# Kernel optimization log

Hardware: AMD Instinct MI355X
Metric: run time of the kernel (lower is better)

Reference implementation:

```python
import jax, jax.numpy as jnp
import numpy as np

MIN_VAL = 1e-10


def integ_exp_trig(lam, theta, t, t0=None):
    # Analytic integrals of exp(lam*s)*cos(theta*s) and exp(lam*s)*sin(theta*s) on [t0, t].
    if t0 is None:
        t0 = jnp.zeros_like(t)
    exps_t = jnp.nan_to_num(jnp.exp(lam * t))
    exps_t0 = jnp.nan_to_num(jnp.exp(lam * t0))
    denom = jnp.square(lam) + jnp.square(theta)
    scale = jnp.sign(denom) / jnp.clip(denom, MIN_VAL)
    cos_t, sin_t = jnp.cos(theta * t), jnp.sin(theta * t)
    cos_t0, sin_t0 = jnp.cos(theta * t0), jnp.sin(theta * t0)
    res_cos = scale * (exps_t * (lam * cos_t + theta * sin_t)
                       - exps_t0 * (lam * cos_t0 + theta * sin_t0))
    res_sin = scale * (exps_t * (lam * sin_t - theta * cos_t)
                       - exps_t0 * (lam * sin_t0 - theta * cos_t0))
    return jnp.nan_to_num(res_cos), jnp.nan_to_num(res_sin)


def esde_predict_complex(X0, X0_var, U, times, Q, lam_real, lam_imag, V_real, V_imag):
    B, n = X0.shape
    m = n // 2
    lam = lam_real + 1j * lam_imag          # [B, m] complex
    V = V_real + 1j * V_imag                # [B, n, m] complex
    X0c = X0[:, :, None]                    # [B, n, 1]

    # Phi(0): exp(0*lam) = 1, so phi_comp = V
    Phi0 = jnp.concatenate([V.real, V.imag], axis=2)        # [B, n, n]
    Phi0_inv = jnp.nan_to_num(jnp.linalg.inv(Phi0))

    init_cond = Phi0_inv @ X0c                               # [B, n, 1]
    init_var = Phi0_inv @ X0_var @ jnp.swapaxes(Phi0_inv, -1, -2)

    # Phi(t)
    et = jnp.exp(times[:, None].astype(lam.dtype) * lam)     # [B, m] complex
    phi = V * et[:, None, :]                                 # right-mult by diag(et)
    Phi = jnp.nan_to_num(jnp.concatenate([phi.real, phi.imag], axis=2))  # [B, n, n]

    Hom = Phi @ init_cond
    Hom_var = Phi @ init_var @ jnp.swapaxes(Phi, -1, -2)
    # force positive diagonal: diag -> |diag|, off-diag unchanged
    eye = jnp.eye(n, dtype=Hom_var.dtype)
    diag_sign = jnp.sign(jnp.diagonal(Hom_var, axis1=-2, axis2=-1))  # [B, n]
    Hom_var = Hom_var * ((1.0 - eye) + eye * diag_sign[:, :, None])

    # ----- particular (control) term: block 2x2 rotation-integral times Phi0_inv @ U
    ext_u = (Phi0_inv @ U[:, :, None]).reshape(B, m, 2)      # interleaved (re, im) pairs
    cos_int, sin_int = integ_exp_trig(-lam.real, lam.imag, times[:, None])  # [B, m]
    li0 = cos_int * ext_u[..., 0] - sin_int * ext_u[..., 1]
    li1 = sin_int * ext_u[..., 0] + cos_int * ext_u[..., 1]
    lambda_int = jnp.stack([li0, li1], axis=-1).reshape(B, n, 1)
    Part = Phi @ lambda_int

    # ----- diffusion variance term
    ext_s = Phi0_inv @ Q @ jnp.swapaxes(Phi0_inv, -1, -2)    # [B, n, n]
    ls = lam[:, None, :] + lam[:, :, None]                   # lam_i + lam_j
    ls_conj = lam[:, None, :] - lam[:, :, None]              # lam_j - lam_i
    t3 = times[:, None, None]
    cos1, sin1 = integ_exp_trig(-ls.real, ls.imag, t3)       # [B, m, m]
    cos2, sin2 = integ_exp_trig(-ls.real, ls_conj.imag, t3)
    vcc = 0.5 * (cos1 + cos2)   # int cos*cos
    vsc = 0.5 * (sin1 + sin2)   # int sin*cos
    vcs = 0.5 * (sin1 - sin2)   # int cos*sin
    vss = 0.5 * (cos2 - cos1)   # int sin*sin
    E = ext_s.reshape(B, m, 2, m, 2)  # interleaved 2x2 block structure
    d11, d12 = E[:, :, 0, :, 0], E[:, :, 0, :, 1]
    d21, d22 = E[:, :, 1, :, 0], E[:, :, 1, :, 1]
    r11 = vcc * d11 - vsc * d21 - vcs * d12 + vss * d22
    r12 = vcs * d11 - vss * d21 + vcc * d12 - vsc * d22
    r21 = vsc * d11 + vcc * d21 - vss * d12 - vcs * d22
    r22 = vss * d11 + vcs * d21 + vsc * d12 + vcc * d22
    row0 = jnp.stack([r11, r12], axis=-1)   # [B, m, m, 2]
    row1 = jnp.stack([r21, r22], axis=-1)
    sig_int = jnp.stack([row0, row1], axis=2).reshape(B, n, n)
    Part_var = Phi @ sig_int @ jnp.swapaxes(Phi, -1, -2)

    return Hom + Part, Hom_var + Part_var


def setup_inputs() -> dict:
    key = jax.random.key(0)
    ks = jax.random.split(key, 9)
    B, n = 65536, 16
    m = n // 2
    X0 = jax.random.normal(ks[0], (B, n), jnp.float32)
    A = jax.random.normal(ks[1], (B, n, n), jnp.float32) * 0.1
    X0_var = A @ jnp.swapaxes(A, -1, -2) + 0.1 * jnp.eye(n, dtype=jnp.float32)
    U = jax.random.normal(ks[2], (B, n), jnp.float32)
    times = jax.random.uniform(ks[3], (B,), jnp.float32, 0.1, 2.0)
    Qa = jax.random.normal(ks[4], (B, n, n), jnp.float32) * 0.1
    Q = Qa @ jnp.swapaxes(Qa, -1, -2)
    lam_real = -jax.random.uniform(ks[5], (B, m), jnp.float32, 0.05, 1.0)
    lam_imag = jax.random.uniform(ks[6], (B, m), jnp.float32, -2.0, 2.0)
    V_real = jax.random.normal(ks[7], (B, n, m), jnp.float32)
    V_imag = jax.random.normal(ks[8], (B, n, m), jnp.float32)
    return {"X0": X0, "X0_var": X0_var, "U": U, "times": times, "Q": Q,
            "lam_real": lam_real, "lam_imag": lam_imag,
            "V_real": V_real, "V_imag": V_imag}


def reference(X0, X0_var, U, times, Q, lam_real, lam_imag, V_real, V_imag):
    return esde_predict_complex(X0, X0_var, U, times, Q,
                                lam_real, lam_imag, V_real, V_imag)
```

## Files before the change

kernel.cpp:

```cpp
#include <hip/hip_runtime.h>
#include <math.h>

#define WSYNC() do { __builtin_amdgcn_wave_barrier(); asm volatile("" ::: "memory"); } while (0)
#define LFENCE() asm volatile("" ::: "memory")

constexpr int FS = 20;

typedef float v2f __attribute__((ext_vector_type(2)));
__device__ inline v2f pkfma(v2f a, v2f b, v2f c) {
  return __builtin_elementwise_fma(a, b, c);
}

struct alignas(16) WaveMem {
  float P[16 * FS];
  float F[16 * FS];
  float W[16 * FS];
  float L1[16 * FS];
  float L4[16 * FS];
  float etr[8], eti[8], lamr[8], lami[8];
  float vx0[16], vu[16], vic[16];
};

__device__ inline float n2n(float v) {
  if (isnan(v)) return 0.0f;
  if (isinf(v)) return v > 0.f ? 3.402823466e38f : -3.402823466e38f;
  return v;
}

__device__ inline float readlane_f(float v, int l) {
  return __int_as_float(__builtin_amdgcn_readlane(__float_as_int(v), l));
}
template<int CTRL>
__device__ inline float dpp_f(float v) {
  return __int_as_float(__builtin_amdgcn_mov_dpp(__float_as_int(v), CTRL, 0xF, 0xF, true));
}

__device__ inline void load16(float out[16], const float* p) {
#pragma unroll
  for (int c = 0; c < 4; ++c) {
    float4 v = *(const float4*)(p + 4 * c);
    out[4*c+0] = v.x; out[4*c+1] = v.y; out[4*c+2] = v.z; out[4*c+3] = v.w;
  }
}

template<bool TRB>
__device__ inline void mmv(float* C, const float* A, const float* Bm,
                           int i16, int jg, bool absdiag = false)
{
  const int j0 = jg << 2;
  float aA[16];
  load16(aA, &A[i16 * FS]);
  float acc[4];
  if (TRB) {
#pragma unroll
    for (int cp = 0; cp < 2; ++cp) {
      float bB0[16], bB1[16];
      load16(bB0, &Bm[(j0 + 2*cp) * FS]);
      load16(bB1, &Bm[(j0 + 2*cp + 1) * FS]);
      v2f s = {0.f, 0.f};
#pragma unroll
      for (int k = 0; k < 16; ++k)
        s = pkfma((v2f){aA[k], aA[k]}, (v2f){bB0[k], bB1[k]}, s);
      acc[2*cp] = s.x; acc[2*cp+1] = s.y;
    }
  } else {
    v2f a01 = {0.f, 0.f}, a23 = {0.f, 0.f};
#pragma unroll
    for (int k = 0; k < 16; ++k) {
      float4 bv = *(const float4*)&Bm[k * FS + j0];
      v2f ad = {aA[k], aA[k]};
      a01 = pkfma(ad, (v2f){bv.x, bv.y}, a01);
      a23 = pkfma(ad, (v2f){bv.z, bv.w}, a23);
    }
    acc[0] = a01.x; acc[1] = a01.y; acc[2] = a23.x; acc[3] = a23.y;
  }
  if (absdiag) {
#pragma unroll
    for (int c = 0; c < 4; ++c) if (i16 == j0 + c) acc[c] = fabsf(acc[c]);
  }
  *(float4*)&C[i16 * FS + j0] = make_float4(acc[0], acc[1], acc[2], acc[3]);
}

__global__ __launch_bounds__(256, 6) void nesde_kernel(
    const float* __restrict__ gX0, const float* __restrict__ gXv,
    const float* __restrict__ gU,  const float* __restrict__ gT,
    const float* __restrict__ gQ,  const float* __restrict__ gLr,
    const float* __restrict__ gLi, const float* __restrict__ gVr,
    const float* __restrict__ gVi, float* __restrict__ gOut0,
    float* __restrict__ gOut1, int B)
{
  __shared__ WaveMem sm[4];
  const int wid  = threadIdx.x >> 6;
  const int lane = threadIdx.x & 63;
  const int b = blockIdx.x * 4 + wid;
  if (b >= B) return;
  WaveMem& S = sm[wid];

  const int r4  = lane >> 2;
  const int q   = lane & 3;
  const int i16 = lane & 15;
  const int jg  = lane >> 4;
  const int j0  = jg << 2;

  const float t = gT[b];

  const float4 xv = *(const float4*)(gXv + (size_t)b * 256 + lane * 4);
  const float4 qv = *(const float4*)(gQ  + (size_t)b * 256 + lane * 4);
  float4 va = make_float4(0.f,0.f,0.f,0.f), vb = va;
  if (q < 2) {
    const float* src = (q == 0) ? gVr : gVi;
    va = *(const float4*)(src + (size_t)b * 128 + r4 * 8);
    vb = *(const float4*)(src + (size_t)b * 128 + r4 * 8 + 4);
  }
  float x0u = 0.f;
  if (q == 2) x0u = gX0[(size_t)b * 16 + r4];
  if (q == 3) x0u = gU [(size_t)b * 16 + r4];

  if (lane < 8) {
    float lr = gLr[(size_t)b * 8 + lane];
    float li = gLi[(size_t)b * 8 + lane];
    S.lamr[lane] = lr; S.lami[lane] = li;
    float e = expf(lr * t);
    float sn, cs; sincosf(li * t, &sn, &cs);
    S.etr[lane] = e * cs;
    S.eti[lane] = e * sn;
  }
  WSYNC();

  float4 vco;
  {
    const int p = lane >> 3, qq = lane & 7;
    float la  = -(S.lamr[p] + S.lamr[qq]);
    float th1 = S.lami[p] + S.lami[qq];
    float th2 = S.lami[qq] - S.lami[p];
    float exps = __expf(la * t);
    float s1, c1, s2, c2;
    __sincosf(th1 * t, &s1, &c1);
    __sincosf(th2 * t, &s2, &c2);
    float den1 = la * la + th1 * th1;
    float sg1 = (den1 > 0.f) ? 1.f : ((den1 < 0.f) ? -1.f : 0.f);
    float sc1 = sg1 / fmaxf(den1, 1e-10f);
    float cos1 = sc1 * (exps * (la * c1 + th1 * s1) - la);
    float sin1 = sc1 * (exps * (la * s1 - th1 * c1) + th1);
    float den2 = la * la + th2 * th2;
    float sg2 = (den2 > 0.f) ? 1.f : ((den2 < 0.f) ? -1.f : 0.f);
    float sc2 = sg2 / fmaxf(den2, 1e-10f);
    float cos2 = sc2 * (exps * (la * c2 + th2 * s2) - la);
    float sin2 = sc2 * (exps * (la * s2 - th2 * c2) + th2);
    vco = make_float4(0.5f * (cos1 + cos2), 0.5f * (sin1 + sin2),
                      0.5f * (sin1 - sin2), 0.5f * (cos2 - cos1));
  }
  {
    const int si = lane >> 2, sj = (lane & 3) * 4;
    *(float4*)&S.L1[si * FS + sj] = xv;
    *(float4*)&S.L4[si * FS + sj] = qv;
  }
  if (q == 2) S.vx0[r4] = x0u;
  if (q == 3) S.vu[r4]  = x0u;

  float myv[8] = { va.x, va.y, va.z, va.w, vb.x, vb.y, vb.z, vb.w };
  float ov[8];
#pragma unroll
  for (int e = 0; e < 8; ++e) ov[e] = __shfl_xor(myv[e], 1);
  if (q < 2) {
    float er[8], ei[8];
#pragma unroll
    for (int e = 0; e < 8; ++e) { er[e] = S.etr[e]; ei[e] = S.eti[e]; }
    float vr[8], vi[8], ph[8];
#pragma unroll
    for (int e = 0; e < 8; ++e) {
      vr[e] = (q == 0) ? myv[e] : ov[e];
      vi[e] = (q == 0) ? ov[e]  : myv[e];
    }
    if (q == 0) {
#pragma unroll
      for (int e = 0; e < 8; ++e) ph[e] = vr[e] * er[e] - vi[e] * ei[e];
      *(float4*)&S.F[r4 * FS + 0] = make_float4(ph[0], ph[1], ph[2], ph[3]);
      *(float4*)&S.F[r4 * FS + 4] = make_float4(ph[4], ph[5], ph[6], ph[7]);
    } else {
#pragma unroll
      for (int e = 0; e < 8; ++e) ph[e] = vr[e] * ei[e] + vi[e] * er[e];
      *(float4*)&S.F[r4 * FS + 8]  = make_float4(ph[0], ph[1], ph[2], ph[3]);
      *(float4*)&S.F[r4 * FS + 12] = make_float4(ph[4], ph[5], ph[6], ph[7]);
    }
  }

  float a[8];
#pragma unroll
  for (int e = 0; e < 8; ++e) {
    float idv = 0.f;
    if (q == 2) idv = (r4 == e)     ? 1.f : 0.f;
    if (q == 3) idv = (r4 == 8 + e) ? 1.f : 0.f;
    a[e] = (q < 2) ? myv[e] : idv;
  }

  unsigned used = 0;
  int myk = 0;
#pragma unroll
  for (int k = 0; k < 16; ++k) {
    const int qk = k >> 3, ek = k & 7;
    float av = a[ek];
    float ck = (qk == 0) ? dpp_f<0x00>(av) : dpp_f<0x55>(av);
    float cand = ((used >> r4) & 1u) ? -1.0f : fabsf(ck);
    float mx = cand;
    mx = fmaxf(mx, dpp_f<0x124>(mx));
    mx = fmaxf(mx, dpp_f<0x128>(mx));
    mx = fmaxf(mx, dpp_f<0x142>(mx));
    mx = fmaxf(mx, dpp_f<0x143>(mx));
    float smx = readlane_f(mx, 63);
    unsigned long long msk = __ballot(cand == smx);
    const int pl4 = (__ffsll((long long)msk) - 1) & 60;
    const bool isp = ((lane & 60) == pl4);
    if (isp) {
      *(float4*)&S.W[q * 8]     = make_float4(a[0], a[1], a[2], a[3]);
      *(float4*)&S.W[q * 8 + 4] = make_float4(a[4], a[5], a[6], a[7]);
    }
    float pval = readlane_f(av, pl4 | qk);
    float pivinv = 1.0f / pval;
    LFENCE();
    float4 r0 = *(const float4*)&S.W[q * 8];
    float4 r1 = *(const float4*)&S.W[q * 8 + 4];
    LFENCE();
    float rr[8] = { r0.x, r0.y, r0.z, r0.w, r1.x, r1.y, r1.z, r1.w };
    const v2f pivd = { pivinv, pivinv };
    const v2f nck  = { -ck, -ck };
#pragma unroll
    for (int e2 = 0; e2 < 4; ++e2) {
      v2f rrp = { rr[2*e2], rr[2*e2+1] };
      v2f sp  = rrp * pivd;
      v2f up  = pkfma(nck, sp, (v2f){ a[2*e2], a[2*e2+1] });
      a[2*e2]   = isp ? sp.x : up.x;
      a[2*e2+1] = isp ? sp.y : up.y;
    }
    used |= 1u << (pl4 >> 2);
    if (isp) myk = k;
  }

  if (q >= 2) {
    const int base = myk * FS + ((q - 2) << 3);
    *(float4*)&S.P[base]     = make_float4(n2n(a[0]), n2n(a[1]), n2n(a[2]), n2n(a[3]));
    *(float4*)&S.P[base + 4] = make_float4(n2n(a[4]), n2n(a[5]), n2n(a[6]), n2n(a[7]));
  }
  WSYNC();

  if (lane < 32) {
    const float* src = (lane < 16) ? S.vx0 : S.vu;
    float sv[16], pA[16];
    load16(pA, &S.P[i16 * FS]);
    load16(sv, src);
    float d = 0.f;
#pragma unroll
    for (int k = 0; k < 16; ++k) d = fmaf(pA[k], sv[k], d);
    if (lane < 16) S.vic[i16] = d; else S.vu[i16] = d;
  }
  WSYNC();
  if (lane < 8) {
    float la = -S.lamr[lane], th = S.lami[lane];
    float exps = expf(la * t);
    float sn, cs; sincosf(th * t, &sn, &cs);
    float denom = la * la + th * th;
    float sgn = (denom > 0.f) ? 1.f : ((denom < 0.f) ? -1.f : 0.f);
    float scale = sgn / fmaxf(denom, 1e-10f);
    float ci = scale * (exps * (la * cs + th * sn) - la);
    float si = scale * (exps * (la * sn - th * cs) + th);
    float e0 = S.vu[2 * lane], e1 = S.vu[2 * lane + 1];
    S.vic[2 * lane]     += ci * e0 - si * e1;
    S.vic[2 * lane + 1] += si * e0 + ci * e1;
  }
  WSYNC();
  if (lane < 16) {
    float fA[16], vv[16];
    load16(fA, &S.F[lane * FS]);
    load16(vv, S.vic);
    float d = 0.f;
#pragma unroll
    for (int k = 0; k < 16; ++k) d = fmaf(fA[k], vv[k], d);
    gOut0[(size_t)b * 16 + lane] = d;
  }
  WSYNC();

  mmv<false>(S.W,  S.P, S.L4, i16, jg);        WSYNC();
  mmv<true >(S.L4, S.W, S.P,  i16, jg);        WSYNC();
  mmv<false>(S.W,  S.F, S.P,  i16, jg);        WSYNC();
  mmv<false>(S.P,  S.W, S.L1, i16, jg);        WSYNC();
  mmv<true >(S.L1, S.P, S.W,  i16, jg, true);  WSYNC();

  {
    const int p2 = i16 >> 1, aa = i16 & 1;
    const int sA = p2 * 8 + (j0 >> 1);
    float4 c0, c1;
    c0.x = __shfl(vco.x, sA);     c0.y = __shfl(vco.y, sA);
    c0.z = __shfl(vco.z, sA);     c0.w = __shfl(vco.w, sA);
    c1.x = __shfl(vco.x, sA + 1); c1.y = __shfl(vco.y, sA + 1);
    c1.z = __shfl(vco.z, sA + 1); c1.w = __shfl(vco.w, sA + 1);
    float4 top = *(const float4*)&S.L4[(2 * p2) * FS + j0];
    float4 bot = *(const float4*)&S.L4[(2 * p2 + 1) * FS + j0];
    float tl[4] = { top.x, top.y, top.z, top.w };
    float bl[4] = { bot.x, bot.y, bot.z, bot.w };
    float r[4];
#pragma unroll
    for (int uu = 0; uu < 4; ++uu) {
      float4 c = (uu < 2) ? c0 : c1;
      const int off = 2 * (uu >> 1);
      float d11 = tl[off], d12 = tl[off + 1];
      float d21 = bl[off], d22 = bl[off + 1];
      const int bb = uu & 1;
      if (aa == 0)
        r[uu] = (bb == 0) ? (c.x * d11 - c.y * d21 - c.z * d12 + c.w * d22)
                          : (c.z * d11 - c.w * d21 + c.x * d12 - c.y * d22);
      else
        r[uu] = (bb == 0) ? (c.y * d11 + c.x * d21 - c.w * d12 - c.z * d22)
                          : (c.w * d11 + c.z * d21 + c.y * d12 + c.x * d22);
    }
    *(float4*)&S.W[i16 * FS + j0] = make_float4(r[0], r[1], r[2], r[3]);
  }
  WSYNC();
  mmv<false>(S.L4, S.F, S.W, i16, jg);         WSYNC();

  {
    float aA[16];
    load16(aA, &S.L4[i16 * FS]);
    float acc[4];
#pragma unroll
    for (int cp = 0; cp < 2; ++cp) {
      float bB0[16], bB1[16];
      load16(bB0, &S.F[(j0 + 2*cp) * FS]);
      load16(bB1, &S.F[(j0 + 2*cp + 1) * FS]);
      v2f s = {0.f, 0.f};
#pragma unroll
      for (int k = 0; k < 16; ++k)
        s = pkfma((v2f){aA[k], aA[k]}, (v2f){bB0[k], bB1[k]}, s);
      acc[2*cp] = s.x; acc[2*cp+1] = s.y;
    }
    float4 hv = *(const float4*)&S.L1[i16 * FS + j0];
    float4 o = make_float4(hv.x + acc[0], hv.y + acc[1], hv.z + acc[2], hv.w + acc[3]);
    *(float4*)&gOut1[(size_t)b * 256 + i16 * 16 + j0] = o;
  }
}

extern "C" void kernel_launch(void* const* d_in, const int* in_sizes, int n_in,
                              void* d_out, int out_size, void* d_ws, size_t ws_size,
                              hipStream_t stream) {
  const float* X0 = (const float*)d_in[0];
  const float* Xv = (const float*)d_in[1];
  const float* U  = (const float*)d_in[2];
  const float* T  = (const float*)d_in[3];
  const float* Q  = (const float*)d_in[4];
  const float* Lr = (const float*)d_in[5];
  const float* Li = (const float*)d_in[6];
  const float* Vr = (const float*)d_in[7];
  const float* Vi = (const float*)d_in[8];
  const int B = in_sizes[3];
  float* out0 = (float*)d_out;
  float* out1 = (float*)d_out + (size_t)B * 16;
  const int blocks = (B + 3) / 4;
  hipLaunchKernelGGL(nesde_kernel, dim3(blocks), dim3(256), 0, stream,
                     X0, Xv, U, T, Q, Lr, Li, Vr, Vi, out0, out1, B);
}
```

Before: 192.3 us.

## Switch matrix inversion to in-place Gauss-Jordan with 4 columns per lane

Rewrites the per-batch 16x16 inverse. Before, each lane carried 8 entries of an augmented [V|I] matrix. Now each of the four lanes in a row group holds 4 columns and the pivot columns are overwritten in place with the inverse. Pivot positions are recorded in packed nibble masks so the columns can be unpermuted at the final scatter. The V load and the Phi construction are reorganised so that all four lanes do equal work. This halves per-lane register use and FMA work in the elimination loop, at the cost of a scattered scalar store at the end.

```diff
diff --git a/kernel.cpp b/kernel.cpp
--- a/kernel.cpp
+++ b/kernel.cpp
@@ -106,11 +106,10 @@
 
   const float4 xv = *(const float4*)(gXv + (size_t)b * 256 + lane * 4);
   const float4 qv = *(const float4*)(gQ  + (size_t)b * 256 + lane * 4);
-  float4 va = make_float4(0.f,0.f,0.f,0.f), vb = va;
-  if (q < 2) {
-    const float* src = (q == 0) ? gVr : gVi;
-    va = *(const float4*)(src + (size_t)b * 128 + r4 * 8);
-    vb = *(const float4*)(src + (size_t)b * 128 + r4 * 8 + 4);
+  float4 v4;
+  {
+    const float* src = (q < 2) ? gVr : gVi;
+    v4 = *(const float4*)(src + (size_t)b * 128 + r4 * 8 + ((q & 1) << 2));
   }
   float x0u = 0.f;
   if (q == 2) x0u = gX0[(size_t)b * 16 + r4];
@@ -158,49 +157,34 @@
   if (q == 2) S.vx0[r4] = x0u;
   if (q == 3) S.vu[r4]  = x0u;
 
-  float myv[8] = { va.x, va.y, va.z, va.w, vb.x, vb.y, vb.z, vb.w };
-  float ov[8];
-#pragma unroll
-  for (int e = 0; e < 8; ++e) ov[e] = __shfl_xor(myv[e], 1);
-  if (q < 2) {
-    float er[8], ei[8];
-#pragma unroll
-    for (int e = 0; e < 8; ++e) { er[e] = S.etr[e]; ei[e] = S.eti[e]; }
-    float vr[8], vi[8], ph[8];
-#pragma unroll
-    for (int e = 0; e < 8; ++e) {
-      vr[e] = (q == 0) ? myv[e] : ov[e];
-      vi[e] = (q == 0) ? ov[e]  : myv[e];
-    }
-    if (q == 0) {
-#pragma unroll
-      for (int e = 0; e < 8; ++e) ph[e] = vr[e] * er[e] - vi[e] * ei[e];
-      *(float4*)&S.F[r4 * FS + 0] = make_float4(ph[0], ph[1], ph[2], ph[3]);
-      *(float4*)&S.F[r4 * FS + 4] = make_float4(ph[4], ph[5], ph[6], ph[7]);
+  float mv[4] = { v4.x, v4.y, v4.z, v4.w };
+  float pvv[4];
+#pragma unroll
+  for (int e = 0; e < 4; ++e) pvv[e] = __shfl_xor(mv[e], 2);
+  {
+    const int cbase = (q & 1) << 2;
+    float er[4], ei[4], ph[4];
+#pragma unroll
+    for (int e = 0; e < 4; ++e) { er[e] = S.etr[cbase + e]; ei[e] = S.eti[cbase + e]; }
+    if (q < 2) {
+#pragma unroll
+      for (int e = 0; e < 4; ++e) ph[e] = mv[e] * er[e] - pvv[e] * ei[e];
     } else {
 #pragma unroll
-      for (int e = 0; e < 8; ++e) ph[e] = vr[e] * ei[e] + vi[e] * er[e];
-      *(float4*)&S.F[r4 * FS + 8]  = make_float4(ph[0], ph[1], ph[2], ph[3]);
-      *(float4*)&S.F[r4 * FS + 12] = make_float4(ph[4], ph[5], ph[6], ph[7]);
-    }
-  }
-
-  float a[8];
-#pragma unroll
-  for (int e = 0; e < 8; ++e) {
-    float idv = 0.f;
-    if (q == 2) idv = (r4 == e)     ? 1.f : 0.f;
-    if (q == 3) idv = (r4 == 8 + e) ? 1.f : 0.f;
-    a[e] = (q < 2) ? myv[e] : idv;
-  }
-
-  unsigned used = 0;
+      for (int e = 0; e < 4; ++e) ph[e] = pvv[e] * ei[e] + mv[e] * er[e];
+    }
+    *(float4*)&S.F[r4 * FS + (q << 2)] = make_float4(ph[0], ph[1], ph[2], ph[3]);
+  }
+
+  float a[4] = { mv[0], mv[1], mv[2], mv[3] };
+  unsigned used = 0, plo = 0, phh = 0;
   int myk = 0;
 #pragma unroll
   for (int k = 0; k < 16; ++k) {
-    const int qk = k >> 3, ek = k & 7;
-    float av = a[ek];
-    float ck = (qk == 0) ? dpp_f<0x00>(av) : dpp_f<0x55>(av);
+    const int kq = k >> 2, ke = k & 3;
+    float av = a[ke];
+    float ck = (kq == 0) ? dpp_f<0x00>(av) : (kq == 1) ? dpp_f<0x55>(av)
+             : (kq == 2) ? dpp_f<0xAA>(av) : dpp_f<0xFF>(av);
     float cand = ((used >> r4) & 1u) ? -1.0f : fabsf(ck);
     float mx = cand;
     mx = fmaxf(mx, dpp_f<0x124>(mx));
@@ -211,35 +195,38 @@
     unsigned long long msk = __ballot(cand == smx);
     const int pl4 = (__ffsll((long long)msk) - 1) & 60;
     const bool isp = ((lane & 60) == pl4);
-    if (isp) {
-      *(float4*)&S.W[q * 8]     = make_float4(a[0], a[1], a[2], a[3]);
-      *(float4*)&S.W[q * 8 + 4] = make_float4(a[4], a[5], a[6], a[7]);
-    }
-    float pval = readlane_f(av, pl4 | qk);
+    if (isp) *(float4*)&S.W[q << 2] = make_float4(a[0], a[1], a[2], a[3]);
+    float pval = readlane_f(av, pl4 | kq);
     float pivinv = 1.0f / pval;
     LFENCE();
-    float4 r0 = *(const float4*)&S.W[q * 8];
-    float4 r1 = *(const float4*)&S.W[q * 8 + 4];
+    float4 rr4 = *(const float4*)&S.W[q << 2];
     LFENCE();
-    float rr[8] = { r0.x, r0.y, r0.z, r0.w, r1.x, r1.y, r1.z, r1.w };
     const v2f pivd = { pivinv, pivinv };
     const v2f nck  = { -ck, -ck };
-#pragma unroll
-    for (int e2 = 0; e2 < 4; ++e2) {
-      v2f rrp = { rr[2*e2], rr[2*e2+1] };
-      v2f sp  = rrp * pivd;
-      v2f up  = pkfma(nck, sp, (v2f){ a[2*e2], a[2*e2+1] });
-      a[2*e2]   = isp ? sp.x : up.x;
-      a[2*e2+1] = isp ? sp.y : up.y;
-    }
+    {
+      v2f sp = (v2f){ rr4.x, rr4.y } * pivd;
+      v2f up = pkfma(nck, sp, (v2f){ a[0], a[1] });
+      a[0] = isp ? sp.x : up.x;
+      a[1] = isp ? sp.y : up.y;
+      v2f sp2 = (v2f){ rr4.z, rr4.w } * pivd;
+      v2f up2 = pkfma(nck, sp2, (v2f){ a[2], a[3] });
+      a[2] = isp ? sp2.x : up2.x;
+      a[3] = isp ? sp2.y : up2.y;
+    }
+    if (q == kq) a[ke] = isp ? pivinv : -(ck * pivinv);
     used |= 1u << (pl4 >> 2);
     if (isp) myk = k;
-  }
-
-  if (q >= 2) {
-    const int base = myk * FS + ((q - 2) << 3);
-    *(float4*)&S.P[base]     = make_float4(n2n(a[0]), n2n(a[1]), n2n(a[2]), n2n(a[3]));
-    *(float4*)&S.P[base + 4] = make_float4(n2n(a[4]), n2n(a[5]), n2n(a[6]), n2n(a[7]));
+    const unsigned p = (unsigned)(pl4 >> 2);
+    if (k < 8) plo |= p << (4 * k); else phh |= p << (4 * (k - 8));
+  }
+
+  {
+#pragma unroll
+    for (int e = 0; e < 4; ++e) {
+      const int c = (q << 2) + e;
+      const unsigned nib = (q < 2) ? (plo >> (4 * c)) : (phh >> (4 * (c - 8)));
+      S.P[myk * FS + (nib & 15u)] = n2n(a[e]);
+    }
   }
   WSYNC();
 
```

Measured after the change: 175.3 us, median of 2. -8.8%, faster.
